# Performance work log

Measured on AMD Instinct MI355X. Metric: run time of the kernel, lower is better.

Reference implementation:

```python
import jax, jax.numpy as jnp
import numpy as np

DIM = 512
HEADS = 8
DIM_HEAD = 64
INNER = HEADS * DIM_HEAD  # 512
SCALE = DIM_HEAD ** -0.5


def setup_inputs() -> dict:
    key = jax.random.key(0)
    k1, k2, k3, k4, k5 = jax.random.split(key, 5)
    B, N = 4, 2048
    x = jax.random.normal(k1, (B, N, DIM), dtype=jnp.float32)
    # LayerNorm params
    ln_gamma = jnp.ones((DIM,), dtype=jnp.float32)
    ln_beta = jnp.zeros((DIM,), dtype=jnp.float32)
    # Linear weights (torch nn.Linear stores [out, in]; we keep [in, out] for x @ W)
    w_qkv = jax.random.normal(k2, (DIM, 3 * INNER), dtype=jnp.float32) * (DIM ** -0.5)
    w_out = jax.random.normal(k3, (INNER, DIM), dtype=jnp.float32) * (INNER ** -0.5)
    return {"x": x, "ln_gamma": ln_gamma, "ln_beta": ln_beta, "w_qkv": w_qkv, "w_out": w_out}


def _layernorm(x, gamma, beta, eps=1e-5):
    mu = jnp.mean(x, axis=-1, keepdims=True)
    var = jnp.var(x, axis=-1, keepdims=True)
    return (x - mu) * jax.lax.rsqrt(var + eps) * gamma + beta


def reference(x, ln_gamma, ln_beta, w_qkv, w_out):
    B, N, _ = x.shape
    h = _layernorm(x, ln_gamma, ln_beta)
    qkv = h @ w_qkv                                   # [B, N, 3*INNER]
    q, k, v = jnp.split(qkv, 3, axis=-1)
    def to_heads(t):
        return t.reshape(B, N, HEADS, DIM_HEAD).transpose(0, 2, 1, 3)  # b h n d
    q, k, v = to_heads(q), to_heads(k), to_heads(v)
    dots = jnp.einsum('bhnd,bhmd->bhnm', q, k) * SCALE
    attn = jax.nn.softmax(dots, axis=-1)
    out = jnp.einsum('bhnm,bhmd->bhnd', attn, v)
    out = out.transpose(0, 2, 1, 3).reshape(B, N, INNER)
    return out @ w_out
```

## Files before the change

kernel.cpp:

```cpp
#include <hip/hip_runtime.h>
#include <hip/hip_bf16.h>

#define B_ 4
#define SEQ 2048
#define DIM_ 512
#define DH 64
#define NQKV 1536
#define ROWS (B_*SEQ)
#define QSCALE 0.1803368801111204f
#define FRAG_PER_BH (SEQ * DH)

typedef short v8s __attribute__((ext_vector_type(8)));
typedef short v4sv __attribute__((ext_vector_type(4)));
typedef float v4f __attribute__((ext_vector_type(4)));
typedef unsigned v4u __attribute__((ext_vector_type(4)));

#define MFMA16(a,b,c) __builtin_amdgcn_mfma_f32_16x16x32_bf16((a),(b),(c),0,0,0)

#if __has_builtin(__builtin_amdgcn_exp2f)
#define EXP2(x) __builtin_amdgcn_exp2f(x)
#else
#define EXP2(x) exp2f(x)
#endif

static __device__ __forceinline__ short f2bf(float f) {
    union { __hip_bfloat16 h; short s; } u;
    u.h = __float2bfloat16(f);
    return u.s;
}

static __device__ __forceinline__ unsigned cvtpk(float lo, float hi) {
    unsigned r;
    asm("v_cvt_pk_bf16_f32 %0, %1, %2" : "=v"(r) : "v"(lo), "v"(hi));
    return r;
}

static __device__ __forceinline__ v8s as_v8s(v4u u) {
    union { v4u u; v8s s; } p;
    p.u = u;
    return p.s;
}

static __device__ __forceinline__ void gll16(const void* g, void* l) {
    __builtin_amdgcn_global_load_lds((const __attribute__((address_space(1))) void*)g,
                                     (__attribute__((address_space(3))) void*)l,
                                     16, 0, 0);
}

__global__ __launch_bounds__(256) void ln_kernel(const float* __restrict__ x,
                                                 const float* __restrict__ gamma,
                                                 const float* __restrict__ beta,
                                                 short* __restrict__ h) {
    int wave = threadIdx.x >> 6;
    int lane = threadIdx.x & 63;
    int row = (blockIdx.x << 2) + wave;
    const float* xr = x + (size_t)row * DIM_ + lane * 8;
    float4 a = *(const float4*)xr;
    float4 b = *(const float4*)(xr + 4);
    float v[8] = {a.x, a.y, a.z, a.w, b.x, b.y, b.z, b.w};
    float s = 0.f, ss = 0.f;
#pragma unroll
    for (int j = 0; j < 8; j++) { s += v[j]; ss += v[j] * v[j]; }
#pragma unroll
    for (int off = 1; off < 64; off <<= 1) {
        s += __shfl_xor(s, off, 64);
        ss += __shfl_xor(ss, off, 64);
    }
    float mean = s * (1.f / DIM_);
    float var = ss * (1.f / DIM_) - mean * mean;
    float rstd = rsqrtf(var + 1e-5f);
    const float* gr = gamma + lane * 8;
    const float* br = beta + lane * 8;
    float4 g0 = *(const float4*)gr, g1 = *(const float4*)(gr + 4);
    float4 b0 = *(const float4*)br, b1 = *(const float4*)(br + 4);
    float gg[8] = {g0.x, g0.y, g0.z, g0.w, g1.x, g1.y, g1.z, g1.w};
    float bb[8] = {b0.x, b0.y, b0.z, b0.w, b1.x, b1.y, b1.z, b1.w};
    v8s o;
#pragma unroll
    for (int j = 0; j < 8; j++) o[j] = f2bf((v[j] - mean) * rstd * gg[j] + bb[j]);
    *(v8s*)(h + (size_t)row * DIM_ + lane * 8) = o;
}

__global__ __launch_bounds__(256) void castw_kernel(const float* __restrict__ w,
                                                    short* __restrict__ wt,
                                                    int K, int Ntot, int scale_cols) {
    __shared__ float tile[64][65];
    int nb = Ntot >> 6;
    int k0 = (blockIdx.x / nb) << 6;
    int n0 = (blockIdx.x % nb) << 6;
    int tc = threadIdx.x & 63;
    int t4 = threadIdx.x >> 6;
#pragma unroll
    for (int i = 0; i < 16; i++) {
        int r = (t4 << 4) + i;
        float val = w[(size_t)(k0 + r) * Ntot + n0 + tc];
        if (n0 + tc < scale_cols) val *= QSCALE;
        tile[r][tc] = val;
    }
    __syncthreads();
#pragma unroll
    for (int i = 0; i < 16; i++) {
        int r = (t4 << 4) + i;
        wt[(size_t)(n0 + r) * K + k0 + tc] = f2bf(tile[tc][r]);
    }
}

template <int MODE>
__global__ __launch_bounds__(256, 3) void gemm_kernel(const short* __restrict__ A,
                                                      const short* __restrict__ Bt,
                                                      short* __restrict__ Qo,
                                                      short* __restrict__ Kf,
                                                      short* __restrict__ Vf,
                                                      float* __restrict__ out,
                                                      int Ntot) {
    __shared__ short lmem[2 * 128 * 64];
    short* lA = lmem;
    short* lB = lmem + 128 * 64;
    int nb = Ntot >> 7;
    int wid = ((int)(blockIdx.x & 7)) * ((int)gridDim.x >> 3) + ((int)blockIdx.x >> 3);
    int m0 = (wid / nb) << 7;
    int n0 = (wid % nb) << 7;
    int t = threadIdx.x;
    int wave = t >> 6, lane = t & 63;
    int ql = lane & 15, grp = lane >> 4;
    int wr = (wave >> 1) << 6, wc = (wave & 1) << 6;
    int srow = lane >> 3;
    int scol = ((lane & 7) ^ srow) << 3;
    const short* Asrc = A + (size_t)(m0 + (wave << 5) + srow) * DIM_ + scol;
    const short* Bsrc = Bt + (size_t)(n0 + (wave << 5) + srow) * DIM_ + scol;
    short* lAw = &lA[(wave << 5) << 6];
    short* lBw = &lB[(wave << 5) << 6];
    int swz = (ql & 7) << 3;
    v4f acc[4][4];
#pragma unroll
    for (int i = 0; i < 4; i++)
#pragma unroll
        for (int j = 0; j < 4; j++)
#pragma unroll
            for (int r = 0; r < 4; r++) acc[i][j][r] = 0.f;

    for (int k0 = 0; k0 < DIM_; k0 += 64) {
#pragma unroll
        for (int i = 0; i < 4; i++) {
            gll16(Asrc + k0 + (size_t)(i << 3) * DIM_, lAw + ((i << 3) << 6));
            gll16(Bsrc + k0 + (size_t)(i << 3) * DIM_, lBw + ((i << 3) << 6));
        }
        __syncthreads();
#pragma unroll
        for (int kk = 0; kk < 64; kk += 32) {
            v8s af[4], bfr[4];
#pragma unroll
            for (int ms = 0; ms < 4; ms++)
                af[ms] = *(const v8s*)&lA[((wr + (ms << 4) + ql) << 6) + ((kk + (grp << 3)) ^ swz)];
#pragma unroll
            for (int ns = 0; ns < 4; ns++)
                bfr[ns] = *(const v8s*)&lB[((wc + (ns << 4) + ql) << 6) + ((kk + (grp << 3)) ^ swz)];
#pragma unroll
            for (int ms = 0; ms < 4; ms++)
#pragma unroll
                for (int ns = 0; ns < 4; ns++)
                    acc[ms][ns] = MFMA16(af[ms], bfr[ns], acc[ms][ns]);
        }
        __syncthreads();
    }
    if (MODE == 1) {
#pragma unroll
        for (int ms = 0; ms < 4; ms++)
#pragma unroll
            for (int ns = 0; ns < 4; ns++)
#pragma unroll
                for (int r = 0; r < 4; r++) {
                    int m = m0 + wr + (ms << 4) + (grp << 2) + r;
                    int n = n0 + wc + (ns << 4) + ql;
                    out[(size_t)m * DIM_ + n] = acc[ms][ns][r];
                }
    } else if (n0 < 512) {
#pragma unroll
        for (int ms = 0; ms < 4; ms++)
#pragma unroll
            for (int ns = 0; ns < 4; ns++)
#pragma unroll
                for (int r = 0; r < 4; r++) {
                    int m = m0 + wr + (ms << 4) + (grp << 2) + r;
                    int n = n0 + wc + (ns << 4) + ql;
                    int head = (n >> 6) & 7;
                    int d = n & 63;
                    int b = m >> 11;
                    int nseq = m & 2047;
                    size_t bh = (size_t)((b << 3) + head);
                    Qo[(bh * SEQ + nseq) * DH + d] = f2bf(acc[ms][ns][r]);
                }
    } else if (n0 < 1024) {
#pragma unroll
        for (int ms = 0; ms < 4; ms++)
#pragma unroll
            for (int ns = 0; ns < 4; ns++)
#pragma unroll
                for (int r = 0; r < 4; r++) {
                    int m = m0 + wr + (ms << 4) + (grp << 2) + r;
                    int n = n0 + wc + (ns << 4) + ql;
                    int head = (n >> 6) & 7;
                    int d = n & 63;
                    int b = m >> 11;
                    int nseq = m & 2047;
                    int tl = nseq >> 6, p = nseq & 63;
                    int pp = (p & 32) | (((p >> 2) & 1) << 4) | (((p >> 4) & 1) << 3)
                           | (((p >> 3) & 1) << 2) | (p & 3);
                    int tt = pp >> 4, qlk = pp & 15;
                    int hh = d >> 5, grpk = (d >> 3) & 3, j = d & 7;
                    size_t bh = (size_t)((b << 3) + head);
                    Kf[bh * FRAG_PER_BH +
                       ((((size_t)(tl * 4 + tt) * 2 + hh) * 64 + grpk * 16 + qlk) << 3) + j] =
                        f2bf(acc[ms][ns][r]);
                }
    } else {
#pragma unroll
        for (int ms = 0; ms < 4; ms++)
#pragma unroll
            for (int ns = 0; ns < 4; ns++) {
                int seq0 = (m0 & 2047) + wr + (ms << 4) + (grp << 2);
                int tl = seq0 >> 6, s = seq0 & 63;
                int g = s >> 5, grpv = (s >> 3) & 3, j0 = s & 7;
                int n = n0 + wc + (ns << 4) + ql;
                int head = (n >> 6) & 7;
                int d = n & 63;
                int ds = d >> 4, qlv = d & 15;
                int b = m0 >> 11;
                size_t bh = (size_t)((b << 3) + head);
                v4sv o;
#pragma unroll
                for (int r = 0; r < 4; r++) o[r] = f2bf(acc[ms][ns][r]);
                *(v4sv*)&Vf[bh * FRAG_PER_BH +
                            ((((size_t)(tl * 2 + g) * 4 + ds) * 64 + grpv * 16 + qlv) << 3) + j0] = o;
            }
    }
}

__global__ __launch_bounds__(512) void attn_kernel(const short* __restrict__ Q,
                                                   const short* __restrict__ Kf,
                                                   const short* __restrict__ Vf,
                                                   short* __restrict__ aout) {
    int tid = threadIdx.x;
    int wave = tid >> 6, lane = tid & 63;
    int ql = lane & 15, grp = lane >> 4;
    int wid = (((int)blockIdx.x & 7) << 5) + ((int)blockIdx.x >> 3);
    int bh = wid >> 3;
    int q0 = (wid & 7) << 8;
    const short* Qb = Q + (size_t)bh * SEQ * DH;
    const short* Kb = Kf + (size_t)bh * FRAG_PER_BH;
    const short* Vb = Vf + (size_t)bh * FRAG_PER_BH;
    int l16 = lane << 3;

    v8s qf[2][2];
#pragma unroll
    for (int qs = 0; qs < 2; qs++) {
        const short* qrow = Qb + (size_t)(q0 + (wave << 5) + (qs << 4) + ql) * DH + (grp << 3);
        qf[qs][0] = *(const v8s*)qrow;
        qf[qs][1] = *(const v8s*)(qrow + 32);
    }

    v4f oacc[2][4];
#pragma unroll
    for (int qs = 0; qs < 2; qs++)
#pragma unroll
        for (int i = 0; i < 4; i++)
#pragma unroll
            for (int r = 0; r < 4; r++) oacc[qs][i][r] = 0.f;
    float plocal[2] = {0.f, 0.f};
    const v4f vzero = {0.f, 0.f, 0.f, 0.f};

    v8s kA[8], kB[8];
#pragma unroll
    for (int f = 0; f < 8; f++) kA[f] = *(const v8s*)&Kb[(f << 9) + l16];

#define ATTN_TILE(T, KC, KN)                                                            \
    {                                                                                   \
        v8s vcur[8];                                                                    \
        _Pragma("unroll")                                                               \
        for (int f = 0; f < 8; f++)                                                     \
            vcur[f] = *(const v8s*)&Vb[((T) << 12) + (f << 9) + l16];                   \
        if ((T) + 1 < SEQ / 64) {                                                       \
            _Pragma("unroll")                                                           \
            for (int f = 0; f < 8; f++)                                                 \
                KN[f] = *(const v8s*)&Kb[(((T) + 1) << 12) + (f << 9) + l16];           \
        }                                                                               \
        v4f sacc[2][4];                                                                 \
        __builtin_amdgcn_s_setprio(1);                                                  \
        _Pragma("unroll")                                                               \
        for (int tt = 0; tt < 4; tt++)                                                  \
            _Pragma("unroll")                                                           \
            for (int qs = 0; qs < 2; qs++) {                                            \
                sacc[qs][tt] = MFMA16(KC[(tt << 1)], qf[qs][0], vzero);                 \
                sacc[qs][tt] = MFMA16(KC[(tt << 1) + 1], qf[qs][1], sacc[qs][tt]);      \
            }                                                                           \
        __builtin_amdgcn_s_setprio(0);                                                  \
        v4u pk[2][2];                                                                   \
        _Pragma("unroll")                                                               \
        for (int qs = 0; qs < 2; qs++)                                                  \
            _Pragma("unroll")                                                           \
            for (int tt = 0; tt < 4; tt++) {                                            \
                float e0 = EXP2(sacc[qs][tt][0]);                                       \
                float e1 = EXP2(sacc[qs][tt][1]);                                       \
                float e2 = EXP2(sacc[qs][tt][2]);                                       \
                float e3 = EXP2(sacc[qs][tt][3]);                                       \
                plocal[qs] += (e0 + e1) + (e2 + e3);                                    \
                pk[qs][tt >> 1][(tt & 1) << 1] = cvtpk(e0, e1);                         \
                pk[qs][tt >> 1][((tt & 1) << 1) + 1] = cvtpk(e2, e3);                   \
            }                                                                           \
        __builtin_amdgcn_s_setprio(1);                                                  \
        _Pragma("unroll")                                                               \
        for (int g = 0; g < 2; g++)                                                     \
            _Pragma("unroll")                                                           \
            for (int qs = 0; qs < 2; qs++) {                                            \
                v8s pf = as_v8s(pk[qs][g]);                                             \
                _Pragma("unroll")                                                       \
                for (int ds = 0; ds < 4; ds++)                                          \
                    oacc[qs][ds] = MFMA16(vcur[(g << 2) + ds], pf, oacc[qs][ds]);       \
            }                                                                           \
        __builtin_amdgcn_s_setprio(0);                                                  \
    }

    for (int t = 0; t < SEQ / 64; t += 2) {
        ATTN_TILE(t, kA, kB);
        ATTN_TILE(t + 1, kB, kA);
    }
#undef ATTN_TILE

    int b = bh >> 3, head = bh & 7;
#pragma unroll
    for (int qs = 0; qs < 2; qs++) {
        float p = plocal[qs];
        p += __shfl_xor(p, 16, 64);
        p += __shfl_xor(p, 32, 64);
        float inv = 1.f / p;
        int n = q0 + (wave << 5) + (qs << 4) + ql;
        size_t rowbase = ((size_t)(b * SEQ + n)) * DIM_ + (head << 6);
#pragma unroll
        for (int ds = 0; ds < 4; ds++) {
            v4sv o;
#pragma unroll
            for (int r = 0; r < 4; r++) o[r] = f2bf(oacc[qs][ds][r] * inv);
            *(v4sv*)&aout[rowbase + (ds << 4) + (grp << 2)] = o;
        }
    }
}

extern "C" void kernel_launch(void* const* d_in, const int* in_sizes, int n_in,
                              void* d_out, int out_size, void* d_ws, size_t ws_size,
                              hipStream_t stream) {
    const float* x = (const float*)d_in[0];
    const float* gamma = (const float*)d_in[1];
    const float* beta = (const float*)d_in[2];
    const float* w_qkv = (const float*)d_in[3];
    const float* w_out = (const float*)d_in[4];
    float* out = (float*)d_out;

    short* ws = (short*)d_ws;
    short* h = ws;
    short* wqkvT = h + (size_t)ROWS * DIM_;
    short* woutT = wqkvT + (size_t)NQKV * DIM_;
    short* Qb = woutT + (size_t)DIM_ * DIM_;
    short* Kfb = Qb + (size_t)32 * SEQ * DH;
    short* Vfb = Kfb + (size_t)32 * SEQ * DH;
    short* aout = Vfb + (size_t)32 * SEQ * DH;

    hipLaunchKernelGGL(ln_kernel, dim3(ROWS / 4), dim3(256), 0, stream, x, gamma, beta, h);
    hipLaunchKernelGGL(castw_kernel, dim3((DIM_ / 64) * (NQKV / 64)), dim3(256), 0, stream,
                       w_qkv, wqkvT, DIM_, NQKV, 512);
    hipLaunchKernelGGL(castw_kernel, dim3((DIM_ / 64) * (DIM_ / 64)), dim3(256), 0, stream,
                       w_out, woutT, DIM_, DIM_, 0);
    hipLaunchKernelGGL((gemm_kernel<0>), dim3((ROWS / 128) * (NQKV / 128)), dim3(256), 0, stream,
                       h, wqkvT, Qb, Kfb, Vfb, (float*)nullptr, NQKV);
    hipLaunchKernelGGL(attn_kernel, dim3(32 * 8), dim3(512), 0, stream, Qb, Kfb, Vfb, aout);
    hipLaunchKernelGGL((gemm_kernel<1>), dim3((ROWS / 128) * (DIM_ / 128)), dim3(256), 0, stream,
                       aout, woutT, (short*)nullptr, (short*)nullptr, (short*)nullptr, out, DIM_);
}
```

Measured before the change: 91.85 us.

## Stage QKV GEMM epilogue through swizzled LDS for vectorized Q/K/V stores

The QKV GEMM epilogue now writes the accumulator tile into LDS with an XOR swizzle, synchronizes, then has each thread emit 16-byte vector stores into the Q, fragment-ordered K and V layouts, replacing scattered 2-byte and 8-byte global stores. The two weight-cast launches are also merged into one kernel that picks its matrix by block index. The intent is to coalesce global writes in the epilogue and drop one launch, at the cost of an extra LDS round-trip and a barrier in the epilogue.

Measured after the change: 89.76 us. -2.3%, faster.

```diff
diff --git a/kernel.cpp b/kernel.cpp
--- a/kernel.cpp
+++ b/kernel.cpp
@@ -81,13 +81,22 @@
     *(v8s*)(h + (size_t)row * DIM_ + lane * 8) = o;
 }
 
-__global__ __launch_bounds__(256) void castw_kernel(const float* __restrict__ w,
-                                                    short* __restrict__ wt,
-                                                    int K, int Ntot, int scale_cols) {
+__global__ __launch_bounds__(256) void castw_kernel(const float* __restrict__ wqkv,
+                                                    const float* __restrict__ wout,
+                                                    short* __restrict__ wqkvT,
+                                                    short* __restrict__ woutT) {
     __shared__ float tile[64][65];
+    const float* w;
+    short* wt;
+    int Ntot, scale_cols, idx;
+    if (blockIdx.x < 192) {
+        w = wqkv; wt = wqkvT; Ntot = NQKV; scale_cols = 512; idx = blockIdx.x;
+    } else {
+        w = wout; wt = woutT; Ntot = DIM_; scale_cols = 0; idx = blockIdx.x - 192;
+    }
     int nb = Ntot >> 6;
-    int k0 = (blockIdx.x / nb) << 6;
-    int n0 = (blockIdx.x % nb) << 6;
+    int k0 = (idx / nb) << 6;
+    int n0 = (idx % nb) << 6;
     int tc = threadIdx.x & 63;
     int t4 = threadIdx.x >> 6;
 #pragma unroll
@@ -101,7 +110,7 @@
 #pragma unroll
     for (int i = 0; i < 16; i++) {
         int r = (t4 << 4) + i;
-        wt[(size_t)(n0 + r) * K + k0 + tc] = f2bf(tile[tc][r]);
+        wt[(size_t)(n0 + r) * DIM_ + k0 + tc] = f2bf(tile[tc][r]);
     }
 }
 
@@ -174,65 +183,80 @@
                     int n = n0 + wc + (ns << 4) + ql;
                     out[(size_t)m * DIM_ + n] = acc[ms][ns][r];
                 }
-    } else if (n0 < 512) {
+    } else if (n0 < 1024) {
+        short* lt = lmem;
 #pragma unroll
         for (int ms = 0; ms < 4; ms++)
 #pragma unroll
+            for (int ns = 0; ns < 4; ns++) {
+                int n_loc = wc + (ns << 4) + ql;
+                int cb = n_loc >> 3, nlo = n_loc & 7;
+#pragma unroll
+                for (int r = 0; r < 4; r++) {
+                    int m_loc = wr + (ms << 4) + (grp << 2) + r;
+                    lt[(m_loc << 7) + (((cb ^ (m_loc & 15)) << 3) | nlo)] = f2bf(acc[ms][ns][r]);
+                }
+            }
+        __syncthreads();
+        int rr = t >> 1, ch = t & 1;
+        int m = m0 + rr;
+        int b = m >> 11, nseq = m & 2047;
+        int mm15 = rr & 15;
+        int head = ((n0 >> 6) + ch) & 7;
+        size_t bh = (size_t)((b << 3) + head);
+        if (n0 < 512) {
+            short* dst = &Qo[(bh * SEQ + nseq) * DH];
+#pragma unroll
+            for (int i = 0; i < 8; i++) {
+                int c = (ch << 3) + i;
+                v8s val = *(const v8s*)&lt[(rr << 7) + ((c ^ mm15) << 3)];
+                *(v8s*)&dst[i << 3] = val;
+            }
+        } else {
+            int tl = nseq >> 6, p = nseq & 63;
+            int pp = (p & 32) | (((p >> 2) & 1) << 4) | (((p >> 4) & 1) << 3)
+                   | (((p >> 3) & 1) << 2) | (p & 3);
+            int tt = pp >> 4, qlk = pp & 15;
+            size_t base = bh * FRAG_PER_BH + (size_t)(tl * 4 + tt) * 1024 + qlk * 8;
+#pragma unroll
+            for (int dc = 0; dc < 8; dc++) {
+                int c = (ch << 3) + dc;
+                v8s val = *(const v8s*)&lt[(rr << 7) + ((c ^ mm15) << 3)];
+                *(v8s*)&Kf[base + ((dc >> 2) << 9) + ((dc & 3) << 7)] = val;
+            }
+        }
+    } else {
+        short* lt = lmem;
+#pragma unroll
+        for (int ms = 0; ms < 4; ms++)
+#pragma unroll
             for (int ns = 0; ns < 4; ns++)
 #pragma unroll
                 for (int r = 0; r < 4; r++) {
-                    int m = m0 + wr + (ms << 4) + (grp << 2) + r;
-                    int n = n0 + wc + (ns << 4) + ql;
-                    int head = (n >> 6) & 7;
-                    int d = n & 63;
-                    int b = m >> 11;
-                    int nseq = m & 2047;
-                    size_t bh = (size_t)((b << 3) + head);
-                    Qo[(bh * SEQ + nseq) * DH + d] = f2bf(acc[ms][ns][r]);
+                    int m_loc = wr + (ms << 4) + (grp << 2) + r;
+                    int n_loc = wc + (ns << 4) + ql;
+                    lt[(n_loc << 7) + (m_loc ^ ((n_loc & 7) << 3))] = f2bf(acc[ms][ns][r]);
                 }
-    } else if (n0 < 1024) {
-#pragma unroll
-        for (int ms = 0; ms < 4; ms++)
-#pragma unroll
-            for (int ns = 0; ns < 4; ns++)
-#pragma unroll
-                for (int r = 0; r < 4; r++) {
-                    int m = m0 + wr + (ms << 4) + (grp << 2) + r;
-                    int n = n0 + wc + (ns << 4) + ql;
-                    int head = (n >> 6) & 7;
-                    int d = n & 63;
-                    int b = m >> 11;
-                    int nseq = m & 2047;
-                    int tl = nseq >> 6, p = nseq & 63;
-                    int pp = (p & 32) | (((p >> 2) & 1) << 4) | (((p >> 4) & 1) << 3)
-                           | (((p >> 3) & 1) << 2) | (p & 3);
-                    int tt = pp >> 4, qlk = pp & 15;
-                    int hh = d >> 5, grpk = (d >> 3) & 3, j = d & 7;
-                    size_t bh = (size_t)((b << 3) + head);
-                    Kf[bh * FRAG_PER_BH +
-                       ((((size_t)(tl * 4 + tt) * 2 + hh) * 64 + grpk * 16 + qlk) << 3) + j] =
-                        f2bf(acc[ms][ns][r]);
-                }
-    } else {
-#pragma unroll
-        for (int ms = 0; ms < 4; ms++)
-#pragma unroll
-            for (int ns = 0; ns < 4; ns++) {
-                int seq0 = (m0 & 2047) + wr + (ms << 4) + (grp << 2);
-                int tl = seq0 >> 6, s = seq0 & 63;
-                int g = s >> 5, grpv = (s >> 3) & 3, j0 = s & 7;
-                int n = n0 + wc + (ns << 4) + ql;
-                int head = (n >> 6) & 7;
-                int d = n & 63;
-                int ds = d >> 4, qlv = d & 15;
-                int b = m0 >> 11;
-                size_t bh = (size_t)((b << 3) + head);
-                v4sv o;
-#pragma unroll
-                for (int r = 0; r < 4; r++) o[r] = f2bf(acc[ms][ns][r]);
-                *(v4sv*)&Vf[bh * FRAG_PER_BH +
-                            ((((size_t)(tl * 2 + g) * 4 + ds) * 64 + grpv * 16 + qlv) << 3) + j0] = o;
-            }
+        __syncthreads();
+        int rrow = t >> 1;
+        int ch = t & 1;
+        int n_glob = n0 + rrow;
+        int head = (n_glob >> 6) & 7;
+        int d = n_glob & 63;
+        int ds = d >> 4, qlv = d & 15;
+        int b = m0 >> 11;
+        size_t bh = (size_t)((b << 3) + head);
+        int swzr = (rrow & 7) << 3;
+#pragma unroll
+        for (int i = 0; i < 8; i++) {
+            int seq_off = (ch << 6) + (i << 3);
+            v8s val = *(const v8s*)&lt[(rrow << 7) + (seq_off ^ swzr)];
+            int seq = (m0 & 2047) + seq_off;
+            int tl = seq >> 6, s = seq & 63;
+            int g = s >> 5, grpv = (s >> 3) & 3;
+            *(v8s*)&Vf[bh * FRAG_PER_BH +
+                       ((((size_t)(tl * 2 + g) * 4 + ds) * 64 + grpv * 16 + qlv) << 3)] = val;
+        }
     }
 }
 
@@ -365,10 +389,8 @@
     short* aout = Vfb + (size_t)32 * SEQ * DH;
 
     hipLaunchKernelGGL(ln_kernel, dim3(ROWS / 4), dim3(256), 0, stream, x, gamma, beta, h);
-    hipLaunchKernelGGL(castw_kernel, dim3((DIM_ / 64) * (NQKV / 64)), dim3(256), 0, stream,
-                       w_qkv, wqkvT, DIM_, NQKV, 512);
-    hipLaunchKernelGGL(castw_kernel, dim3((DIM_ / 64) * (DIM_ / 64)), dim3(256), 0, stream,
-                       w_out, woutT, DIM_, DIM_, 0);
+    hipLaunchKernelGGL(castw_kernel, dim3(256), dim3(256), 0, stream,
+                       w_qkv, w_out, wqkvT, woutT);
     hipLaunchKernelGGL((gemm_kernel<0>), dim3((ROWS / 128) * (NQKV / 128)), dim3(256), 0, stream,
                        h, wqkvT, Qb, Kfb, Vfb, (float*)nullptr, NQKV);
     hipLaunchKernelGGL(attn_kernel, dim3(32 * 8), dim3(512), 0, stream, Qb, Kfb, Vfb, aout);
```
